# Kernel tuning notes

Measured on AMD Instinct MI355X. Metric: run time of the kernel, lower is better.

Reference implementation:

```python
import jax, jax.numpy as jnp
import numpy as np

N = 16      # manifold_dim
H = 128     # hidden_dim
B = 256     # batch
EPS = 1e-6


def setup_inputs() -> dict:
    key = jax.random.key(0)
    ks = jax.random.split(key, 14)
    def w(k, shape):
        fan_in = shape[0]
        return jax.random.uniform(k, shape, jnp.float32, -1.0, 1.0) / np.sqrt(fan_in)
    return {
        "points": jax.random.normal(ks[0], (B, N), jnp.float32),
        # metric network: N -> H -> N*N
        "mW1": w(ks[1], (N, H)), "mb1": jnp.zeros((H,), jnp.float32),
        "mW2": w(ks[2], (H, N * N)), "mb2": jnp.zeros((N * N,), jnp.float32),
        # christoffel network: 3 -> H -> 1
        "cW1": w(ks[3], (3, H)), "cb1": jnp.zeros((H,), jnp.float32),
        "cW2": w(ks[4], (H, 1)), "cb2": jnp.zeros((1,), jnp.float32),
        # ricci network: 4N -> 2H -> N*N
        "rW1": w(ks[5], (4 * N, 2 * H)), "rb1": jnp.zeros((2 * H,), jnp.float32),
        "rW2": w(ks[6], (2 * H, N * N)), "rb2": jnp.zeros((N * N,), jnp.float32),
    }


def reference(points, mW1, mb1, mW2, mb2, cW1, cb1, cW2, cb2, rW1, rb1, rW2, rb2):
    b = points.shape[0]
    n = N
    # ---- metric: (b, n, n) ----
    mh = jax.nn.relu(points @ mW1 + mb1)
    metric = (mh @ mW2 + mb2).reshape(b, n, n)
    metric = metric + EPS * jnp.eye(n, dtype=metric.dtype)
    metric = 0.5 * (metric + jnp.swapaxes(metric, -2, -1))

    # ---- christoffel: vectorized over all (i,j,k) triples ----
    # inputs per triple: [metric_ij, metric_jk, metric_ki]
    m_ij = jnp.broadcast_to(metric[:, :, :, None], (b, n, n, n))
    m_jk = jnp.broadcast_to(metric[:, None, :, :], (b, n, n, n))
    mT = jnp.swapaxes(metric, -2, -1)  # mT[b,i,k] = metric[b,k,i]
    m_ki = jnp.broadcast_to(mT[:, :, None, :], (b, n, n, n))
    ch_in = jnp.stack([m_ij, m_jk, m_ki], axis=-1)        # (b,n,n,n,3)
    ch_h = jnp.tanh(ch_in @ cW1 + cb1)                    # (b,n,n,n,H)
    christoffel = (ch_h @ cW2 + cb2)[..., 0]              # (b,n,n,n)

    # ---- ricci: vectorized over all (i,j) pairs ----
    p_b = jnp.broadcast_to(points[:, None, None, :], (b, n, n, n))
    m_i = jnp.broadcast_to(metric[:, :, None, :], (b, n, n, n))
    m_j = jnp.broadcast_to(metric[:, None, :, :], (b, n, n, n))
    r_in = jnp.concatenate([p_b, m_i, m_j, christoffel], axis=-1)  # (b,n,n,4n)
    r_h = jax.nn.relu(r_in @ rW1 + rb1)                   # (b,n,n,2H)
    r_out = (r_h @ rW2 + rb2).reshape(b, n, n, n, n)      # (b,i,j,n,n)
    r_out = 0.5 * (r_out + jnp.swapaxes(r_out, -1, -2))
    ricci = r_out.sum(axis=(1, 2)) / (n * n)              # (b,n,n)
    return ricci
```

## Files before the change

kernel.cpp:

```cpp
#include <hip/hip_runtime.h>
#include <hip/hip_bf16.h>

#define NDIM 16
#define HDIM 128
#define BATCH 256
#define EPS_D 1e-6f

__global__ __launch_bounds__(256) void metric_proj_kernel(
    const float* __restrict__ points,
    const float* __restrict__ mW1, const float* __restrict__ mb1,
    const float* __restrict__ mW2, const float* __restrict__ mb2,
    const float* __restrict__ rW1, const float* __restrict__ rb1,
    float* __restrict__ metric,
    float* __restrict__ A1, float* __restrict__ Mi, float* __restrict__ Mj) {
  int b = blockIdx.x;
  int t = threadIdx.x;
  __shared__ float p[16];
  __shared__ float mh[128];
  __shared__ float raw[256];
  __shared__ float M[256];
  if (t < 16) p[t] = points[b * 16 + t];
  __syncthreads();
  if (t < 128) {
    float acc = mb1[t];
#pragma unroll
    for (int k = 0; k < 16; ++k) acc = fmaf(p[k], mW1[k * 128 + t], acc);
    mh[t] = fmaxf(acc, 0.f);
  }
  __syncthreads();
  {
    float acc = mb2[t];
#pragma unroll 8
    for (int h = 0; h < 128; ++h) acc = fmaf(mh[h], mW2[h * 256 + t], acc);
    raw[t] = acc;
  }
  __syncthreads();
  {
    int i = t >> 4, j = t & 15;
    float v = 0.5f * (raw[i * 16 + j] + raw[j * 16 + i]);
    if (i == j) v += EPS_D;
    M[t] = v;
    metric[b * 256 + t] = v;
  }
  __syncthreads();
  {
    int h = t;
    float wB[16], wC[16];
#pragma unroll
    for (int c = 0; c < 16; ++c) {
      wB[c] = rW1[(16 + c) * 256 + h];
      wC[c] = rW1[(32 + c) * 256 + h];
    }
    float a = rb1[h];
#pragma unroll
    for (int r = 0; r < 16; ++r) a = fmaf(p[r], rW1[r * 256 + h], a);
    A1[b * 256 + h] = a;
#pragma unroll 2
    for (int i = 0; i < 16; ++i) {
      float mi = 0.f, mj = 0.f;
#pragma unroll
      for (int c = 0; c < 16; ++c) {
        float m = M[i * 16 + c];
        mi = fmaf(m, wB[c], mi);
        mj = fmaf(m, wC[c], mj);
      }
      Mi[(b * 16 + i) * 256 + h] = mi;
      Mj[(b * 16 + i) * 256 + h] = mj;
    }
  }
}

__global__ __launch_bounds__(128) void chr_kernel(
    const float* __restrict__ metric,
    const float* __restrict__ cW1, const float* __restrict__ cb1,
    const float* __restrict__ cW2, const float* __restrict__ cb2,
    const float* __restrict__ rW1,
    const float* __restrict__ A1, const float* __restrict__ Mi,
    const float* __restrict__ Mj,
    float* __restrict__ H2i) {
  int bi = blockIdx.x;
  int b = bi >> 4, i = bi & 15;
  int t = threadIdx.x;
  __shared__ float M[256];
  __shared__ float4 q[128];
  __shared__ float w2[128];
  __shared__ float ch[256];
  M[t] = metric[b * 256 + t];
  M[t + 128] = metric[b * 256 + t + 128];
  {
    const float S = 2.8853900817779268f;
    q[t] = make_float4(S * cW1[t], S * cW1[128 + t], S * cW1[256 + t],
                       S * cb1[t]);
    w2[t] = cW2[t];
  }
  __syncthreads();

  {
    int j0 = t >> 4, k0 = t & 15;
    int j1 = j0 + 8, k1 = k0;
    float x00 = M[i * 16 + j0], x01 = M[j0 * 16 + k0], x02 = M[k0 * 16 + i];
    float x10 = M[i * 16 + j1], x11 = M[j1 * 16 + k1], x12 = M[k1 * 16 + i];
    float c2 = cb2[0];
    float acc0 = c2, acc1 = c2;
#pragma unroll 4
    for (int h = 0; h < 128; ++h) {
      float4 Q = q[h];
      float w = w2[h];
      float pre0 = fmaf(x00, Q.x, fmaf(x01, Q.y, fmaf(x02, Q.z, Q.w)));
      float pre1 = fmaf(x10, Q.x, fmaf(x11, Q.y, fmaf(x12, Q.z, Q.w)));
      float e0 = __builtin_amdgcn_exp2f(pre0);
      float e1 = __builtin_amdgcn_exp2f(pre1);
      float r0 = __builtin_amdgcn_rcpf(e0 + 1.f);
      float r1 = __builtin_amdgcn_rcpf(e1 + 1.f);
      float th0 = fmaf(-2.f, r0, 1.f);
      float th1 = fmaf(-2.f, r1, 1.f);
      acc0 = fmaf(th0, w, acc0);
      acc1 = fmaf(th1, w, acc1);
    }
    ch[t] = acc0;
    ch[t + 128] = acc1;
  }
  __syncthreads();

  {
    int h0 = t, h1 = t + 128;
    float rc0[16], rc1[16];
#pragma unroll
    for (int kk = 0; kk < 16; ++kk) {
      rc0[kk] = rW1[(48 + kk) * 256 + h0];
      rc1[kk] = rW1[(48 + kk) * 256 + h1];
    }
    float base0 = A1[b * 256 + h0] + Mi[bi * 256 + h0];
    float base1 = A1[b * 256 + h1] + Mi[bi * 256 + h1];
    float hacc0 = 0.f, hacc1 = 0.f;
#pragma unroll 2
    for (int jj = 0; jj < 16; ++jj) {
      float cp0 = 0.f, cp1 = 0.f;
#pragma unroll
      for (int kk = 0; kk < 16; ++kk) {
        float c = ch[jj * 16 + kk];
        cp0 = fmaf(c, rc0[kk], cp0);
        cp1 = fmaf(c, rc1[kk], cp1);
      }
      float mj0 = Mj[(b * 16 + jj) * 256 + h0];
      float mj1 = Mj[(b * 16 + jj) * 256 + h1];
      hacc0 += fmaxf(base0 + mj0 + cp0, 0.f);
      hacc1 += fmaxf(base1 + mj1 + cp1, 0.f);
    }
    H2i[bi * 256 + h0] = hacc0;
    H2i[bi * 256 + h1] = hacc1;
  }
}

__global__ __launch_bounds__(256) void final_kernel(
    const float* __restrict__ H2i,
    const float* __restrict__ rW2, const float* __restrict__ rb2,
    float* __restrict__ out) {
  int b = blockIdx.x;
  int t = threadIdx.x;
  __shared__ float G[256];
  __shared__ float T[256];
  float g = 0.f;
#pragma unroll
  for (int i = 0; i < 16; ++i) g += H2i[(b * 16 + i) * 256 + t];
  G[t] = g;
  __syncthreads();
  float acc = 256.f * rb2[t];
#pragma unroll 8
  for (int h = 0; h < 256; ++h) acc = fmaf(G[h], rW2[h * 256 + t], acc);
  T[t] = acc * (1.f / 256.f);
  __syncthreads();
  int k = t >> 4, l = t & 15;
  out[b * 256 + t] = 0.5f * (T[k * 16 + l] + T[l * 16 + k]);
}

extern "C" void kernel_launch(void* const* d_in, const int* in_sizes, int n_in,
                              void* d_out, int out_size, void* d_ws, size_t ws_size,
                              hipStream_t stream) {
  const float* points = (const float*)d_in[0];
  const float* mW1 = (const float*)d_in[1];
  const float* mb1 = (const float*)d_in[2];
  const float* mW2 = (const float*)d_in[3];
  const float* mb2 = (const float*)d_in[4];
  const float* cW1 = (const float*)d_in[5];
  const float* cb1 = (const float*)d_in[6];
  const float* cW2 = (const float*)d_in[7];
  const float* cb2 = (const float*)d_in[8];
  const float* rW1 = (const float*)d_in[9];
  const float* rb1 = (const float*)d_in[10];
  const float* rW2 = (const float*)d_in[11];
  const float* rb2 = (const float*)d_in[12];
  float* out = (float*)d_out;

  float* ws = (float*)d_ws;
  float* metric = ws;
  float* A1 = metric + 65536;
  float* Mi = A1 + 65536;
  float* Mj = Mi + 1048576;
  float* H2i = Mj + 1048576;

  metric_proj_kernel<<<BATCH, 256, 0, stream>>>(points, mW1, mb1, mW2, mb2,
                                                rW1, rb1, metric, A1, Mi, Mj);
  chr_kernel<<<BATCH * NDIM, 128, 0, stream>>>(metric, cW1, cb1, cW2, cb2, rW1,
                                               A1, Mi, Mj, H2i);
  final_kernel<<<BATCH, 256, 0, stream>>>(H2i, rW2, rb2, out);
}
```

Baseline: 145.7 us.

## Process four i-rows per block with one wave each, reducing via atomics

```diff
diff --git a/kernel.cpp b/kernel.cpp
--- a/kernel.cpp
+++ b/kernel.cpp
@@ -12,13 +12,15 @@
     const float* __restrict__ mW2, const float* __restrict__ mb2,
     const float* __restrict__ rW1, const float* __restrict__ rb1,
     float* __restrict__ metric,
-    float* __restrict__ A1, float* __restrict__ Mi, float* __restrict__ Mj) {
+    float* __restrict__ A1, float* __restrict__ Mi, float* __restrict__ Mj,
+    float* __restrict__ G) {
   int b = blockIdx.x;
   int t = threadIdx.x;
   __shared__ float p[16];
   __shared__ float mh[128];
   __shared__ float raw[256];
   __shared__ float M[256];
+  G[b * 256 + t] = 0.f;
   if (t < 16) p[t] = points[b * 16 + t];
   __syncthreads();
   if (t < 128) {
@@ -70,108 +72,126 @@
   }
 }
 
-__global__ __launch_bounds__(128) void chr_kernel(
+__global__ __launch_bounds__(256, 4) void chr_kernel(
     const float* __restrict__ metric,
     const float* __restrict__ cW1, const float* __restrict__ cb1,
     const float* __restrict__ cW2, const float* __restrict__ cb2,
     const float* __restrict__ rW1,
     const float* __restrict__ A1, const float* __restrict__ Mi,
     const float* __restrict__ Mj,
-    float* __restrict__ H2i) {
-  int bi = blockIdx.x;
-  int b = bi >> 4, i = bi & 15;
+    float* __restrict__ G) {
+  int blk = blockIdx.x;
+  int b = blk >> 2, g = blk & 3;
   int t = threadIdx.x;
+  int w = t >> 6, l = t & 63;
+  int i = g * 4 + w;
+  int bi = b * 16 + i;
   __shared__ float M[256];
-  __shared__ float4 q[128];
-  __shared__ float w2[128];
-  __shared__ float ch[256];
+  __shared__ float4 z[128];
+  __shared__ float4 w2p[32];
+  __shared__ float4 ch4[256];
+  float* chf = (float*)ch4;
   M[t] = metric[b * 256 + t];
-  M[t + 128] = metric[b * 256 + t + 128];
-  {
+  if (t < 128) {
     const float S = 2.8853900817779268f;
-    q[t] = make_float4(S * cW1[t], S * cW1[128 + t], S * cW1[256 + t],
+    z[t] = make_float4(S * cW1[t], S * cW1[128 + t], S * cW1[256 + t],
                        S * cb1[t]);
-    w2[t] = cW2[t];
-  }
-  __syncthreads();
-
-  {
-    int j0 = t >> 4, k0 = t & 15;
-    int j1 = j0 + 8, k1 = k0;
-    float x00 = M[i * 16 + j0], x01 = M[j0 * 16 + k0], x02 = M[k0 * 16 + i];
-    float x10 = M[i * 16 + j1], x11 = M[j1 * 16 + k1], x12 = M[k1 * 16 + i];
+  } else {
+    ((float*)w2p)[t - 128] = cW2[t - 128];
+  }
+  __syncthreads();
+
+  {
+    float x0[4], x1[4], x2[4], acc[4];
     float c2 = cb2[0];
-    float acc0 = c2, acc1 = c2;
-#pragma unroll 4
-    for (int h = 0; h < 128; ++h) {
-      float4 Q = q[h];
-      float w = w2[h];
-      float pre0 = fmaf(x00, Q.x, fmaf(x01, Q.y, fmaf(x02, Q.z, Q.w)));
-      float pre1 = fmaf(x10, Q.x, fmaf(x11, Q.y, fmaf(x12, Q.z, Q.w)));
-      float e0 = __builtin_amdgcn_exp2f(pre0);
-      float e1 = __builtin_amdgcn_exp2f(pre1);
-      float r0 = __builtin_amdgcn_rcpf(e0 + 1.f);
-      float r1 = __builtin_amdgcn_rcpf(e1 + 1.f);
-      float th0 = fmaf(-2.f, r0, 1.f);
-      float th1 = fmaf(-2.f, r1, 1.f);
-      acc0 = fmaf(th0, w, acc0);
-      acc1 = fmaf(th1, w, acc1);
-    }
-    ch[t] = acc0;
-    ch[t + 128] = acc1;
-  }
-  __syncthreads();
-
-  {
-    int h0 = t, h1 = t + 128;
-    float rc0[16], rc1[16];
+#pragma unroll
+    for (int m = 0; m < 4; ++m) {
+      int jk = l + 64 * m;
+      int j = jk >> 4, k = jk & 15;
+      x0[m] = M[i * 16 + j];
+      x1[m] = M[j * 16 + k];
+      x2[m] = M[k * 16 + i];
+      acc[m] = c2;
+    }
+    for (int h = 0; h < 128; h += 4) {
+      float4 W2 = w2p[h >> 2];
+      float w2u[4] = {W2.x, W2.y, W2.z, W2.w};
+#pragma unroll
+      for (int u = 0; u < 4; ++u) {
+        float4 Q = z[h + u];
+#pragma unroll
+        for (int m = 0; m < 4; ++m) {
+          float pre = fmaf(x0[m], Q.x, fmaf(x1[m], Q.y, fmaf(x2[m], Q.z, Q.w)));
+          float e = __builtin_amdgcn_exp2f(pre);
+          float r = __builtin_amdgcn_rcpf(e + 1.f);
+          acc[m] = fmaf(w2u[u], fmaf(-2.f, r, 1.f), acc[m]);
+        }
+      }
+    }
+#pragma unroll
+    for (int m = 0; m < 4; ++m) chf[w * 256 + l + 64 * m] = acc[m];
+  }
+
+  {
+    float rc[4][16];
 #pragma unroll
     for (int kk = 0; kk < 16; ++kk) {
-      rc0[kk] = rW1[(48 + kk) * 256 + h0];
-      rc1[kk] = rW1[(48 + kk) * 256 + h1];
-    }
-    float base0 = A1[b * 256 + h0] + Mi[bi * 256 + h0];
-    float base1 = A1[b * 256 + h1] + Mi[bi * 256 + h1];
-    float hacc0 = 0.f, hacc1 = 0.f;
-#pragma unroll 2
+#pragma unroll
+      for (int m = 0; m < 4; ++m)
+        rc[m][kk] = rW1[(48 + kk) * 256 + l + 64 * m];
+    }
+    float base[4], hacc[4];
+#pragma unroll
+    for (int m = 0; m < 4; ++m) {
+      int h = l + 64 * m;
+      base[m] = A1[b * 256 + h] + Mi[bi * 256 + h];
+      hacc[m] = 0.f;
+    }
     for (int jj = 0; jj < 16; ++jj) {
-      float cp0 = 0.f, cp1 = 0.f;
-#pragma unroll
-      for (int kk = 0; kk < 16; ++kk) {
-        float c = ch[jj * 16 + kk];
-        cp0 = fmaf(c, rc0[kk], cp0);
-        cp1 = fmaf(c, rc1[kk], cp1);
+      float4 c0 = ch4[w * 64 + jj * 4 + 0];
+      float4 c1 = ch4[w * 64 + jj * 4 + 1];
+      float4 c2v = ch4[w * 64 + jj * 4 + 2];
+      float4 c3 = ch4[w * 64 + jj * 4 + 3];
+      float cc[16] = {c0.x, c0.y, c0.z, c0.w, c1.x, c1.y, c1.z, c1.w,
+                      c2v.x, c2v.y, c2v.z, c2v.w, c3.x, c3.y, c3.z, c3.w};
+#pragma unroll
+      for (int m = 0; m < 4; ++m) {
+        float cp = 0.f;
+#pragma unroll
+        for (int kk = 0; kk < 16; ++kk) cp = fmaf(cc[kk], rc[m][kk], cp);
+        float mj = Mj[(b * 16 + jj) * 256 + l + 64 * m];
+        hacc[m] += fmaxf(base[m] + mj + cp, 0.f);
       }
-      float mj0 = Mj[(b * 16 + jj) * 256 + h0];
-      float mj1 = Mj[(b * 16 + jj) * 256 + h1];
-      hacc0 += fmaxf(base0 + mj0 + cp0, 0.f);
-      hacc1 += fmaxf(base1 + mj1 + cp1, 0.f);
-    }
-    H2i[bi * 256 + h0] = hacc0;
-    H2i[bi * 256 + h1] = hacc1;
+    }
+#pragma unroll
+    for (int m = 0; m < 4; ++m)
+      atomicAdd(&G[b * 256 + l + 64 * m], hacc[m]);
   }
 }
 
 __global__ __launch_bounds__(256) void final_kernel(
-    const float* __restrict__ H2i,
+    const float* __restrict__ G,
     const float* __restrict__ rW2, const float* __restrict__ rb2,
     float* __restrict__ out) {
   int b = blockIdx.x;
   int t = threadIdx.x;
-  __shared__ float G[256];
+  __shared__ float4 Gs[64];
   __shared__ float T[256];
-  float g = 0.f;
-#pragma unroll
-  for (int i = 0; i < 16; ++i) g += H2i[(b * 16 + i) * 256 + t];
-  G[t] = g;
+  if (t < 64) Gs[t] = ((const float4*)(G + b * 256))[t];
   __syncthreads();
   float acc = 256.f * rb2[t];
-#pragma unroll 8
-  for (int h = 0; h < 256; ++h) acc = fmaf(G[h], rW2[h * 256 + t], acc);
+#pragma unroll 4
+  for (int h4 = 0; h4 < 64; ++h4) {
+    float4 gg = Gs[h4];
+    acc = fmaf(gg.x, rW2[(h4 * 4 + 0) * 256 + t], acc);
+    acc = fmaf(gg.y, rW2[(h4 * 4 + 1) * 256 + t], acc);
+    acc = fmaf(gg.z, rW2[(h4 * 4 + 2) * 256 + t], acc);
+    acc = fmaf(gg.w, rW2[(h4 * 4 + 3) * 256 + t], acc);
+  }
   T[t] = acc * (1.f / 256.f);
   __syncthreads();
-  int k = t >> 4, l = t & 15;
-  out[b * 256 + t] = 0.5f * (T[k * 16 + l] + T[l * 16 + k]);
+  int k = t >> 4, lcol = t & 15;
+  out[b * 256 + t] = 0.5f * (T[k * 16 + lcol] + T[lcol * 16 + k]);
 }
 
 extern "C" void kernel_launch(void* const* d_in, const int* in_sizes, int n_in,
@@ -197,11 +217,11 @@
   float* A1 = metric + 65536;
   float* Mi = A1 + 65536;
   float* Mj = Mi + 1048576;
-  float* H2i = Mj + 1048576;
+  float* G = Mj + 1048576;
 
   metric_proj_kernel<<<BATCH, 256, 0, stream>>>(points, mW1, mb1, mW2, mb2,
-                                                rW1, rb1, metric, A1, Mi, Mj);
-  chr_kernel<<<BATCH * NDIM, 128, 0, stream>>>(metric, cW1, cb1, cW2, cb2, rW1,
-                                               A1, Mi, Mj, H2i);
-  final_kernel<<<BATCH, 256, 0, stream>>>(H2i, rW2, rb2, out);
-}
+                                                rW1, rb1, metric, A1, Mi, Mj, G);
+  chr_kernel<<<BATCH * 4, 256, 0, stream>>>(metric, cW1, cb1, cW2, cb2, rW1,
+                                            A1, Mi, Mj, G);
+  final_kernel<<<BATCH, 256, 0, stream>>>(G, rW2, rb2, out);
+}
```

New measurement: 143.6 us. Within noise of the previous version (-1.4%).
